# Kernel tuning notes

Hardware: AMD Instinct MI355X
Metric: run time of the kernel (lower is better)

## Reference

```python
import jax, jax.numpy as jnp
import numpy as np

B, S, D = 1, 2048, 4096
H, HK, HD = 32, 8, 128  # query heads, kv heads, head dim
T_CACHE = 2048
N_REP = H // HK


def setup_inputs() -> dict:
    key = jax.random.key(0)
    ks = jax.random.split(key, 8)
    x = jax.random.normal(ks[0], (B, S, D), dtype=jnp.float32)
    # multiplicative rope factor, broadcast over head axis
    rope = jax.random.uniform(ks[1], (1, S, 1, HD), dtype=jnp.float32, minval=-1.0, maxval=1.0)
    cache_k = jax.random.normal(ks[2], (B, T_CACHE, HK, HD), dtype=jnp.float32)
    cache_v = jax.random.normal(ks[3], (B, T_CACHE, HK, HD), dtype=jnp.float32)
    wq = jax.random.normal(ks[4], (D, H * HD), dtype=jnp.float32) * 0.02
    wk = jax.random.normal(ks[5], (D, HK * HD), dtype=jnp.float32) * 0.02
    wv = jax.random.normal(ks[6], (D, HK * HD), dtype=jnp.float32) * 0.02
    wo = jax.random.normal(ks[7], (H * HD, D), dtype=jnp.float32) * 0.02
    # mask: [1, 1, S, T_CACHE + S]; attend freely to cache, causal within new chunk
    neg = np.float32(-1e9)
    causal = np.triu(np.full((S, S), neg, dtype=np.float32), k=1)
    mask = np.concatenate([np.zeros((S, T_CACHE), dtype=np.float32), causal], axis=1)
    mask = jnp.asarray(mask)[None, None, :, :]
    return {"x": x, "rope": rope, "mask": mask, "cache_k": cache_k,
            "cache_v": cache_v, "wq": wq, "wk": wk, "wv": wv, "wo": wo}


def reference(x, rope, mask, cache_k, cache_v, wq, wk, wv, wo):
    b, s, _ = x.shape
    scale = 1.0 / np.sqrt(HD).astype(np.float32)
    xq = (x @ wq).reshape(b, s, H, HD) * rope          # [b, s, H, hd]
    xk = (x @ wk).reshape(b, s, HK, HD) * rope         # [b, s, HK, hd]
    xv = (x @ wv).reshape(b, s, HK, HD)
    keys = jnp.concatenate([cache_k, xk], axis=1)      # [b, t, HK, hd]
    vals = jnp.concatenate([cache_v, xv], axis=1)
    keys = jnp.repeat(keys, N_REP, axis=2)             # GQA repeat -> [b, t, H, hd]
    vals = jnp.repeat(vals, N_REP, axis=2)
    scores = jnp.einsum('bshd,bthd->bhst', xq, keys) * scale
    scores = scores + mask
    probs = jax.nn.softmax(scores.astype(jnp.float32), axis=-1).astype(xq.dtype)
    out = jnp.einsum('bhst,bthd->bshd', probs, vals).reshape(b, s, H * HD)
    return out @ wo
```

## Files before the change

### kernel.cpp

```cpp
#include <hip/hip_runtime.h>

typedef unsigned short u16;
typedef unsigned int   u32;
typedef short  s16x8 __attribute__((ext_vector_type(8)));
typedef float  f32x4 __attribute__((ext_vector_type(4)));

__device__ __forceinline__ u16 f2bf(float f) {
    union { float f; u32 i; } x; x.f = f;
    u32 r = x.i + 0x7FFFu + ((x.i >> 16) & 1u);
    return (u16)(r >> 16);
}

__device__ __forceinline__ void gld16(const void* g, void* l) {
    __builtin_amdgcn_global_load_lds((const __attribute__((address_space(1))) void*)g,
                                     (__attribute__((address_space(3))) void*)l,
                                     16, 0, 0);
}

__global__ __launch_bounds__(256)
void cast_bf16(const float* __restrict__ in, u16* __restrict__ out, int n4) {
    int g = blockIdx.x * 256 + threadIdx.x;
    if (g >= n4) return;
    float4 v = ((const float4*)in)[g];
    ushort4 o; o.x = f2bf(v.x); o.y = f2bf(v.y); o.z = f2bf(v.z); o.w = f2bf(v.w);
    ((ushort4*)out)[g] = o;
}

__global__ __launch_bounds__(256)
void tconv(const float* __restrict__ B, u16* __restrict__ Bt, int K, int N) {
    __shared__ float T[32][33];
    int n0 = blockIdx.x * 32, k0 = blockIdx.y * 32;
    int t = threadIdx.x;
    int r = t >> 3, c4 = (t & 7) * 4;
    float4 v = *(const float4*)&B[(size_t)(k0 + r) * N + n0 + c4];
    T[r][c4 + 0] = v.x; T[r][c4 + 1] = v.y; T[r][c4 + 2] = v.z; T[r][c4 + 3] = v.w;
    __syncthreads();
    ushort4 o;
    o.x = f2bf(T[c4 + 0][r]); o.y = f2bf(T[c4 + 1][r]);
    o.z = f2bf(T[c4 + 2][r]); o.w = f2bf(T[c4 + 3][r]);
    *(ushort4*)&Bt[(size_t)(n0 + r) * K + k0 + c4] = o;
}

__global__ __launch_bounds__(256)
void kcache_conv(const float* __restrict__ ck, u16* __restrict__ Kc) {
    int g = blockIdx.x * 256 + threadIdx.x;
    int d = (g & 31) * 4, kh = (g >> 5) & 7, t = g >> 8;
    float4 v = *(const float4*)&ck[(size_t)t * 1024 + kh * 128 + d];
    ushort4 o; o.x = f2bf(v.x); o.y = f2bf(v.y); o.z = f2bf(v.z); o.w = f2bf(v.w);
    *(ushort4*)&Kc[(size_t)kh * 524288 + (size_t)t * 128 + d] = o;
}

__global__ __launch_bounds__(256)
void vcache_conv(const float* __restrict__ cv, u16* __restrict__ Vt) {
    __shared__ float T[32][33];
    int t0 = blockIdx.x * 32, d0 = blockIdx.y * 32, kh = blockIdx.z;
    int t = threadIdx.x;
    int r = t >> 3, c4 = (t & 7) * 4;
    float4 v = *(const float4*)&cv[(size_t)(t0 + r) * 1024 + kh * 128 + d0 + c4];
    T[r][c4 + 0] = v.x; T[r][c4 + 1] = v.y; T[r][c4 + 2] = v.z; T[r][c4 + 3] = v.w;
    __syncthreads();
    ushort4 o;
    o.x = f2bf(T[c4 + 0][r]); o.y = f2bf(T[c4 + 1][r]);
    o.z = f2bf(T[c4 + 2][r]); o.w = f2bf(T[c4 + 3][r]);
    *(ushort4*)&Vt[(size_t)(kh * 128 + d0 + r) * 4096 + t0 + c4] = o;
}

__device__ __forceinline__ void gemm_core(const u16* __restrict__ A,
                                          const u16* __restrict__ Bt,
                                          int K, int m0,
                                          u16* As, u16* Bs, f32x4 acc[4][4])
{
    const int tid = threadIdx.x;
    const int lane = tid & 63, w = tid >> 6;
    const int quad = lane >> 4, l15 = lane & 15;
    const int mw = (w >> 1) * 64, nw = (w & 1) * 64;
    const int lrow = tid >> 2;
    const int lcol = ((tid & 3) ^ (lrow & 3)) * 8;
    const int rsw = l15 & 3;

    for (int k0 = 0; k0 < K; k0 += 32) {
        __syncthreads();
        gld16(A  + (size_t)(m0 +      lrow) * K + k0 + lcol, &As[w * 512]);
        gld16(A  + (size_t)(m0 + 64 + lrow) * K + k0 + lcol, &As[2048 + w * 512]);
        gld16(Bt + (size_t)(           lrow) * K + k0 + lcol, &Bs[w * 512]);
        gld16(Bt + (size_t)(      64 + lrow) * K + k0 + lcol, &Bs[2048 + w * 512]);
        __syncthreads();
        s16x8 af[4], bf[4];
        #pragma unroll
        for (int i = 0; i < 4; ++i)
            af[i] = *(const s16x8*)&As[(mw + i * 16 + l15) * 32 + (quad ^ rsw) * 8];
        #pragma unroll
        for (int j = 0; j < 4; ++j)
            bf[j] = *(const s16x8*)&Bs[(nw + j * 16 + l15) * 32 + (quad ^ rsw) * 8];
        #pragma unroll
        for (int i = 0; i < 4; ++i)
            #pragma unroll
            for (int j = 0; j < 4; ++j)
                acc[i][j] = __builtin_amdgcn_mfma_f32_16x16x32_bf16(
                    af[i], bf[j], acc[i][j], 0, 0, 0);
    }
}

__global__ __launch_bounds__(256, 2)
void gemm_qkv(const u16* __restrict__ A, const u16* __restrict__ Wq,
              const u16* __restrict__ Wk, const u16* __restrict__ Wv,
              u16* __restrict__ Qw, u16* __restrict__ Kc, u16* __restrict__ Vt,
              const float* __restrict__ rope)
{
    __shared__ u16 As[128 * 32];
    __shared__ u16 Bs[128 * 32];
    const int m0 = blockIdx.y * 128, n0 = blockIdx.x * 128;

    const u16* Bt;
    if (n0 < 4096)       Bt = Wq + (size_t)n0 * 4096;
    else if (n0 < 5120)  Bt = Wk + (size_t)(n0 - 4096) * 4096;
    else                 Bt = Wv + (size_t)(n0 - 5120) * 4096;

    f32x4 acc[4][4];
    #pragma unroll
    for (int i = 0; i < 4; ++i)
        #pragma unroll
        for (int j = 0; j < 4; ++j) acc[i][j] = (f32x4)0.f;

    gemm_core(A, Bt, 4096, m0, As, Bs, acc);

    const int lane = threadIdx.x & 63, w = threadIdx.x >> 6;
    const int quad = lane >> 4, l15 = lane & 15;
    const int mw = (w >> 1) * 64, nw = (w & 1) * 64;

    #pragma unroll
    for (int i = 0; i < 4; ++i) {
        #pragma unroll
        for (int j = 0; j < 4; ++j) {
            int mm = m0 + mw + i * 16 + quad * 4;
            int nn = n0 + nw + j * 16 + l15;
            if (nn < 4096) {
                #pragma unroll
                for (int r = 0; r < 4; ++r)
                    Qw[(size_t)(mm + r) * 4096 + nn] =
                        f2bf(acc[i][j][r] * rope[(size_t)(mm + r) * 128 + (nn & 127)]
                             * 0.08838834764831845f);
            } else if (nn < 5120) {
                #pragma unroll
                for (int r = 0; r < 4; ++r)
                    Kc[(size_t)((nn - 4096) >> 7) * 524288
                       + (size_t)(2048 + mm + r) * 128 + (nn & 127)] =
                        f2bf(acc[i][j][r] * rope[(size_t)(mm + r) * 128 + (nn & 127)]);
            } else {
                ushort4 o;
                o.x = f2bf(acc[i][j][0]); o.y = f2bf(acc[i][j][1]);
                o.z = f2bf(acc[i][j][2]); o.w = f2bf(acc[i][j][3]);
                *(ushort4*)&Vt[(size_t)(nn - 5120) * 4096 + 2048 + mm] = o;
            }
        }
    }
}

__global__ __launch_bounds__(256, 2)
void gemm_wo(const u16* __restrict__ A, const u16* __restrict__ Bt,
             float* __restrict__ C)
{
    __shared__ u16 As[128 * 32];
    __shared__ u16 Bs[128 * 32];
    const int m0 = blockIdx.y * 128, n0 = blockIdx.x * 128;

    f32x4 acc[4][4];
    #pragma unroll
    for (int i = 0; i < 4; ++i)
        #pragma unroll
        for (int j = 0; j < 4; ++j) acc[i][j] = (f32x4)0.f;

    gemm_core(A, Bt + (size_t)n0 * 4096, 4096, m0, As, Bs, acc);

    const int lane = threadIdx.x & 63, w = threadIdx.x >> 6;
    const int quad = lane >> 4, l15 = lane & 15;
    const int mw = (w >> 1) * 64, nw = (w & 1) * 64;

    #pragma unroll
    for (int i = 0; i < 4; ++i)
        #pragma unroll
        for (int j = 0; j < 4; ++j) {
            int mm = m0 + mw + i * 16 + quad * 4;
            int nn = n0 + nw + j * 16 + l15;
            #pragma unroll
            for (int r = 0; r < 4; ++r)
                C[(size_t)(mm + r) * 4096 + nn] = acc[i][j][r];
        }
}

__global__ __launch_bounds__(256, 4)
void attn_mfma(const u16* __restrict__ Qw, const u16* __restrict__ Kc,
               const u16* __restrict__ Vt, u16* __restrict__ AO)
{
    __shared__ u16 Ks[2][32 * 128];
    __shared__ u16 Vs[2][128 * 32];
    __shared__ u16 Pb[64 * 40];
    __shared__ float Ls[2][64];

    const int tid = threadIdx.x;
    const int lane = tid & 63, w = tid >> 6;
    const int quad = lane >> 4, l15 = lane & 15;

    const int bid = blockIdx.x + 32 * blockIdx.y;
    const int kh = bid & 7;
    const int inner = bid >> 3;
    const int h = kh * 4 + (inner & 3);
    const int q0 = (inner >> 2) * 64;

    const int kw = w & 1, qw = w >> 1;
    const size_t kvb = (size_t)kh * 524288;

    s16x8 qreg[2][4];
    #pragma unroll
    for (int n = 0; n < 2; ++n)
        #pragma unroll
        for (int ks = 0; ks < 4; ++ks)
            qreg[n][ks] = *(const s16x8*)&Qw[(size_t)(q0 + qw * 32 + n * 16 + l15) * 4096
                                             + h * 128 + ks * 32 + quad * 8];

    f32x4 o[2][4];
    #pragma unroll
    for (int m = 0; m < 2; ++m)
        #pragma unroll
        for (int n = 0; n < 4; ++n) o[m][n] = (f32x4)0.f;
    float lacc[2] = {0.f, 0.f};

    const int krow = tid >> 4, kcol = ((tid & 15) ^ (krow & 15)) * 8;
    const int vrow = tid >> 2, vcol = ((tid & 3) ^ ((vrow >> 1) & 3)) * 8;

    const u16* kpg = Kc + kvb + (size_t)krow * 128 + kcol;
    const u16* vpg = Vt + kvb + (size_t)vrow * 4096 + vcol;

    const int kend = 2112 + q0;

    #pragma unroll
    for (int i = 0; i < 2; ++i)
        gld16(kpg + i * 2048, &Ks[0][i * 2048 + w * 512]);
    #pragma unroll
    for (int i = 0; i < 2; ++i)
        gld16(vpg + (size_t)i * 262144, &Vs[0][i * 2048 + w * 512]);

    int cur = 0;
    for (int t0 = 0; t0 < kend; t0 += 32, cur ^= 1) {
        __syncthreads();

        const int t1 = t0 + 32;
        if (t1 < kend) {
            #pragma unroll
            for (int i = 0; i < 2; ++i)
                gld16(kpg + (size_t)t1 * 128 + i * 2048,
                      &Ks[cur ^ 1][i * 2048 + w * 512]);
            #pragma unroll
            for (int i = 0; i < 2; ++i)
                gld16(vpg + (size_t)i * 262144 + t1,
                      &Vs[cur ^ 1][i * 2048 + w * 512]);
        }

        f32x4 sc[2];
        sc[0] = (f32x4)0.f; sc[1] = (f32x4)0.f;
        #pragma unroll
        for (int ks = 0; ks < 4; ++ks) {
            int kc8 = (((ks * 4 + quad) ^ l15) & 15) * 8;
            s16x8 kf = *(const s16x8*)&Ks[cur][(kw * 16 + l15) * 128 + kc8];
            sc[0] = __builtin_amdgcn_mfma_f32_16x16x32_bf16(kf, qreg[0][ks], sc[0], 0, 0, 0);
            sc[1] = __builtin_amdgcn_mfma_f32_16x16x32_bf16(kf, qreg[1][ks], sc[1], 0, 0, 0);
        }

        const bool maskt = (t0 + 31 > 2048 + q0);
        #pragma unroll
        for (int n2 = 0; n2 < 2; ++n2) {
            float e0 = __expf(sc[n2][0]);
            float e1 = __expf(sc[n2][1]);
            float e2 = __expf(sc[n2][2]);
            float e3 = __expf(sc[n2][3]);
            if (maskt) {
                int key = t0 + kw * 16 + quad * 4;
                int qv  = q0 + qw * 32 + n2 * 16 + l15;
                if (key + 0 >= 2048 && key + 0 - 2048 > qv) e0 = 0.f;
                if (key + 1 >= 2048 && key + 1 - 2048 > qv) e1 = 0.f;
                if (key + 2 >= 2048 && key + 2 - 2048 > qv) e2 = 0.f;
                if (key + 3 >= 2048 && key + 3 - 2048 > qv) e3 = 0.f;
            }
            lacc[n2] += (e0 + e1) + (e2 + e3);
            uint2 pk;
            pk.x = (u32)f2bf(e0) | ((u32)f2bf(e1) << 16);
            pk.y = (u32)f2bf(e2) | ((u32)f2bf(e3) << 16);
            *(uint2*)&Pb[(qw * 32 + n2 * 16 + l15) * 40 + kw * 16 + quad * 4] = pk;
        }

        asm volatile("s_waitcnt lgkmcnt(0)" ::: "memory");
        __builtin_amdgcn_s_barrier();
        asm volatile("" ::: "memory");

        s16x8 vf[2];
        #pragma unroll
        for (int m = 0; m < 2; ++m) {
            int vr = w * 32 + m * 16 + l15;
            int vc = (quad ^ ((vr >> 1) & 3)) * 8;
            vf[m] = *(const s16x8*)&Vs[cur][vr * 32 + vc];
        }
        #pragma unroll
        for (int n = 0; n < 4; ++n) {
            s16x8 pf = *(const s16x8*)&Pb[(n * 16 + l15) * 40 + quad * 8];
            o[0][n] = __builtin_amdgcn_mfma_f32_16x16x32_bf16(vf[0], pf, o[0][n], 0, 0, 0);
            o[1][n] = __builtin_amdgcn_mfma_f32_16x16x32_bf16(vf[1], pf, o[1][n], 0, 0, 0);
        }
    }

    lacc[0] += __shfl_xor(lacc[0], 16); lacc[0] += __shfl_xor(lacc[0], 32);
    lacc[1] += __shfl_xor(lacc[1], 16); lacc[1] += __shfl_xor(lacc[1], 32);
    if (lane < 16) {
        Ls[kw][qw * 32 +      lane] = lacc[0];
        Ls[kw][qw * 32 + 16 + lane] = lacc[1];
    }
    __syncthreads();

    #pragma unroll
    for (int n = 0; n < 4; ++n) {
        int qq = n * 16 + l15;
        float inv = 1.f / (Ls[0][qq] + Ls[1][qq]);
        #pragma unroll
        for (int m = 0; m < 2; ++m) {
            ushort4 ov;
            ov.x = f2bf(o[m][n][0] * inv);
            ov.y = f2bf(o[m][n][1] * inv);
            ov.z = f2bf(o[m][n][2] * inv);
            ov.w = f2bf(o[m][n][3] * inv);
            *(ushort4*)&AO[(size_t)(q0 + qq) * 4096 + h * 128
                           + w * 32 + m * 16 + quad * 4] = ov;
        }
    }
}

extern "C" void kernel_launch(void* const* d_in, const int* in_sizes, int n_in,
                              void* d_out, int out_size, void* d_ws, size_t ws_size,
                              hipStream_t stream)
{
    const float* x      = (const float*)d_in[0];
    const float* rope   = (const float*)d_in[1];
    const float* cacheK = (const float*)d_in[3];
    const float* cacheV = (const float*)d_in[4];
    const float* wq     = (const float*)d_in[5];
    const float* wk     = (const float*)d_in[6];
    const float* wv     = (const float*)d_in[7];
    const float* wo     = (const float*)d_in[8];
    float* out = (float*)d_out;

    u16* xb = (u16*)d_ws;
    u16* W0 = xb + (size_t)8388608;
    u16* W1 = W0 + (size_t)16777216;
    u16* Qw = W1 + (size_t)4194304;
    u16* Kc = Qw + (size_t)8388608;
    u16* Vt = Kc + (size_t)4194304;
    u16* AO = Vt + (size_t)4194304;
    u16* Wv = AO;

    dim3 blk(256);
    cast_bf16<<<dim3(8192), blk, 0, stream>>>(x, xb, 2097152);
    tconv<<<dim3(128, 128), blk, 0, stream>>>(wq, W0, 4096, 4096);
    tconv<<<dim3(32, 128), blk, 0, stream>>>(wk, W1, 4096, 1024);
    tconv<<<dim3(32, 128), blk, 0, stream>>>(wv, Wv, 4096, 1024);
    gemm_qkv<<<dim3(48, 16), blk, 0, stream>>>(xb, W0, W1, Wv, Qw, Kc, Vt, rope);
    kcache_conv<<<dim3(2048), blk, 0, stream>>>(cacheK, Kc);
    vcache_conv<<<dim3(64, 4, 8), blk, 0, stream>>>(cacheV, Vt);
    attn_mfma<<<dim3(32, 32), blk, 0, stream>>>(Qw, Kc, Vt, AO);
    tconv<<<dim3(128, 128), blk, 0, stream>>>(wo, W0, 4096, 4096);
    gemm_wo<<<dim3(32, 16), blk, 0, stream>>>(AO, W0, out);
}
```

Measured before the change: 601.2 us.

## Software-pipeline attention loop to drop mid-iteration barrier, delaying PV by one tile

Restructures the attention inner loop so the P·V product for tile t-1 is computed in iteration t, using double-buffered P in LDS. This removes the second block barrier per iteration, leaving one sync per tile, and lets V loads for the current tile overlap with QK and softmax. It also swizzles the P buffer instead of padding it, uses the packed v_cvt_pk_bf16_f32 instruction for bf16 conversion, and reuses K LDS for the row-sum reduction. The cost is extra LDS for the second P buffer, a peeled final PV step, and more complex buffer rotation.

New measurement: 592.9 us. About the same (-1.4%).

```diff
diff --git a/kernel.cpp b/kernel.cpp
--- a/kernel.cpp
+++ b/kernel.cpp
@@ -192,10 +192,9 @@
 void attn_mfma(const u16* __restrict__ Qw, const u16* __restrict__ Kc,
                const u16* __restrict__ Vt, u16* __restrict__ AO)
 {
-    __shared__ u16 Ks[2][32 * 128];
-    __shared__ u16 Vs[2][128 * 32];
-    __shared__ u16 Pb[64 * 40];
-    __shared__ float Ls[2][64];
+    __shared__ u16 KsBuf[2][32 * 128];
+    __shared__ u16 VsBuf[2][128 * 32];
+    __shared__ u16 PbBuf[2][64 * 32];
 
     const int tid = threadIdx.x;
     const int lane = tid & 63, w = tid >> 6;
@@ -233,35 +232,43 @@
 
     const int kend = 2112 + q0;
 
-    #pragma unroll
-    for (int i = 0; i < 2; ++i)
-        gld16(kpg + i * 2048, &Ks[0][i * 2048 + w * 512]);
-    #pragma unroll
-    for (int i = 0; i < 2; ++i)
-        gld16(vpg + (size_t)i * 262144, &Vs[0][i * 2048 + w * 512]);
-
-    int cur = 0;
-    for (int t0 = 0; t0 < kend; t0 += 32, cur ^= 1) {
+    u16* ks_rd = &KsBuf[0][0]; u16* ks_st = &KsBuf[1][0];
+    u16* vs_rd = &VsBuf[1][0]; u16* vs_st = &VsBuf[0][0];
+    u16* pb_wr = &PbBuf[0][0]; u16* pb_rd = &PbBuf[1][0];
+
+    auto PV = [&](const u16* vs, const u16* pb) {
+        int vr0 = w * 32 + l15;
+        int vr1 = w * 32 + 16 + l15;
+        s16x8 vf0 = *(const s16x8*)&vs[vr0 * 32 + (quad ^ ((vr0 >> 1) & 3)) * 8];
+        s16x8 vf1 = *(const s16x8*)&vs[vr1 * 32 + (quad ^ ((vr1 >> 1) & 3)) * 8];
+        #pragma unroll
+        for (int n = 0; n < 4; ++n) {
+            int q = n * 16 + l15;
+            s16x8 pf = *(const s16x8*)&pb[q * 32 + ((quad ^ (q & 3)) * 8)];
+            o[0][n] = __builtin_amdgcn_mfma_f32_16x16x32_bf16(vf0, pf, o[0][n], 0, 0, 0);
+            o[1][n] = __builtin_amdgcn_mfma_f32_16x16x32_bf16(vf1, pf, o[1][n], 0, 0, 0);
+        }
+    };
+
+    gld16(kpg,        &ks_rd[w * 512]);
+    gld16(kpg + 2048, &ks_rd[2048 + w * 512]);
+
+    for (int t0 = 0; t0 < kend; t0 += 32) {
         __syncthreads();
 
-        const int t1 = t0 + 32;
-        if (t1 < kend) {
-            #pragma unroll
-            for (int i = 0; i < 2; ++i)
-                gld16(kpg + (size_t)t1 * 128 + i * 2048,
-                      &Ks[cur ^ 1][i * 2048 + w * 512]);
-            #pragma unroll
-            for (int i = 0; i < 2; ++i)
-                gld16(vpg + (size_t)i * 262144 + t1,
-                      &Vs[cur ^ 1][i * 2048 + w * 512]);
-        }
+        if (t0 + 32 < kend) {
+            gld16(kpg + (size_t)(t0 + 32) * 128,        &ks_st[w * 512]);
+            gld16(kpg + (size_t)(t0 + 32) * 128 + 2048, &ks_st[2048 + w * 512]);
+        }
+        gld16(vpg + t0,          &vs_st[w * 512]);
+        gld16(vpg + 262144 + t0, &vs_st[2048 + w * 512]);
 
         f32x4 sc[2];
         sc[0] = (f32x4)0.f; sc[1] = (f32x4)0.f;
         #pragma unroll
         for (int ks = 0; ks < 4; ++ks) {
             int kc8 = (((ks * 4 + quad) ^ l15) & 15) * 8;
-            s16x8 kf = *(const s16x8*)&Ks[cur][(kw * 16 + l15) * 128 + kc8];
+            s16x8 kf = *(const s16x8*)&ks_rd[(kw * 16 + l15) * 128 + kc8];
             sc[0] = __builtin_amdgcn_mfma_f32_16x16x32_bf16(kf, qreg[0][ks], sc[0], 0, 0, 0);
             sc[1] = __builtin_amdgcn_mfma_f32_16x16x32_bf16(kf, qreg[1][ks], sc[1], 0, 0, 0);
         }
@@ -282,43 +289,39 @@
                 if (key + 3 >= 2048 && key + 3 - 2048 > qv) e3 = 0.f;
             }
             lacc[n2] += (e0 + e1) + (e2 + e3);
-            uint2 pk;
-            pk.x = (u32)f2bf(e0) | ((u32)f2bf(e1) << 16);
-            pk.y = (u32)f2bf(e2) | ((u32)f2bf(e3) << 16);
-            *(uint2*)&Pb[(qw * 32 + n2 * 16 + l15) * 40 + kw * 16 + quad * 4] = pk;
-        }
-
-        asm volatile("s_waitcnt lgkmcnt(0)" ::: "memory");
-        __builtin_amdgcn_s_barrier();
-        asm volatile("" ::: "memory");
-
-        s16x8 vf[2];
-        #pragma unroll
-        for (int m = 0; m < 2; ++m) {
-            int vr = w * 32 + m * 16 + l15;
-            int vc = (quad ^ ((vr >> 1) & 3)) * 8;
-            vf[m] = *(const s16x8*)&Vs[cur][vr * 32 + vc];
-        }
-        #pragma unroll
-        for (int n = 0; n < 4; ++n) {
-            s16x8 pf = *(const s16x8*)&Pb[(n * 16 + l15) * 40 + quad * 8];
-            o[0][n] = __builtin_amdgcn_mfma_f32_16x16x32_bf16(vf[0], pf, o[0][n], 0, 0, 0);
-            o[1][n] = __builtin_amdgcn_mfma_f32_16x16x32_bf16(vf[1], pf, o[1][n], 0, 0, 0);
-        }
-    }
-
+            u32 p0, p1;
+            asm("v_cvt_pk_bf16_f32 %0, %1, %2" : "=v"(p0) : "v"(e0), "v"(e1));
+            asm("v_cvt_pk_bf16_f32 %0, %1, %2" : "=v"(p1) : "v"(e2), "v"(e3));
+            int q = qw * 32 + n2 * 16 + l15;
+            uint2 pk; pk.x = p0; pk.y = p1;
+            *(uint2*)&pb_wr[q * 32 + (((2 * kw + (quad >> 1)) ^ (q & 3)) * 8)
+                            + (quad & 1) * 4] = pk;
+        }
+
+        if (t0) PV(vs_rd, pb_rd);
+
+        u16* tp;
+        tp = ks_rd; ks_rd = ks_st; ks_st = tp;
+        tp = vs_rd; vs_rd = vs_st; vs_st = tp;
+        tp = pb_rd; pb_rd = pb_wr; pb_wr = tp;
+    }
+
+    __syncthreads();
+    PV(vs_rd, pb_rd);
+
+    float* Ls = (float*)&KsBuf[0][0];
     lacc[0] += __shfl_xor(lacc[0], 16); lacc[0] += __shfl_xor(lacc[0], 32);
     lacc[1] += __shfl_xor(lacc[1], 16); lacc[1] += __shfl_xor(lacc[1], 32);
     if (lane < 16) {
-        Ls[kw][qw * 32 +      lane] = lacc[0];
-        Ls[kw][qw * 32 + 16 + lane] = lacc[1];
+        Ls[kw * 64 + qw * 32 +      lane] = lacc[0];
+        Ls[kw * 64 + qw * 32 + 16 + lane] = lacc[1];
     }
     __syncthreads();
 
     #pragma unroll
     for (int n = 0; n < 4; ++n) {
         int qq = n * 16 + l15;
-        float inv = 1.f / (Ls[0][qq] + Ls[1][qq]);
+        float inv = 1.f / (Ls[qq] + Ls[64 + qq]);
         #pragma unroll
         for (int m = 0; m < 2; ++m) {
             ushort4 ov;
```
